# Kernel optimization log

Measured on AMD Instinct MI355X. Metric: run time of the kernel, lower is better.

The kernel has to match this reference:

```python
import jax, jax.numpy as jnp
import numpy as np

# Grid / solver constants (from init_kwargs)
N = 512        # grid is N x N
H = 1.0        # grid spacing h
IX, JX = 256, 256  # source cell indices
NITER = 1100   # Jacobi iterations; > 2*N so the wavefront fully converges
BIG = 1e10     # 'infinity' init for travel times


def setup_inputs() -> dict:
    key = jax.random.key(0)
    # positive slowness field in [0.5, 1.5)
    f = 0.5 + jax.random.uniform(key, (N, N), dtype=jnp.float32)
    return {"f": f}


def _solve(f):
    """Solve |grad u| = f with u(IX,JX)=0 via Godunov upwind Jacobi iteration.

    Each iteration applies the standard fast-sweeping local update in parallel
    to all cells and takes the pointwise min with the current u; this converges
    to the same viscosity-solution fixed point as sequential sweeping.
    """
    fh = f * H  # [N, N]
    u0 = jnp.full(f.shape, BIG, dtype=f.dtype).at[IX, JX].set(0.0)

    def step(u, _):
        up = jnp.pad(u, 1, constant_values=BIG)
        # one-sided upwind neighbor minima along each axis
        a = jnp.minimum(up[:-2, 1:-1], up[2:, 1:-1])   # i-direction
        b = jnp.minimum(up[1:-1, :-2], up[1:-1, 2:])   # j-direction
        d = jnp.abs(a - b)
        # Godunov update: 1D update if |a-b| >= f*h, else 2D quadratic root
        u_new = jnp.where(
            d >= fh,
            jnp.minimum(a, b) + fh,
            0.5 * (a + b + jnp.sqrt(jnp.maximum(2.0 * fh * fh - d * d, 0.0))),
        )
        u = jnp.minimum(u, u_new).at[IX, JX].set(0.0)
        return u, None

    u, _ = jax.lax.scan(jax.checkpoint(step), u0, None, length=NITER)
    return u


def reference(f):
    return _solve(f)
```

## Files before the change

### kernel.cpp

```cpp
#include <hip/hip_runtime.h>


#define NG     512
#define TS     16
#define BIGV   1e10f
#define SRC_I  256
#define SRC_J  256
#define KIN    16
#define ROUNDS 60
#define LSTR   24

#define GLB_LD(p)    __hip_atomic_load((p),      __ATOMIC_RELAXED, __HIP_MEMORY_SCOPE_AGENT)
#define GLB_ST(p, x) __hip_atomic_store((p), (x), __ATOMIC_RELAXED, __HIP_MEMORY_SCOPE_AGENT)

__device__ __forceinline__ float dpp_shr1(float x, float edge) {
    return __int_as_float(__builtin_amdgcn_update_dpp(
        __float_as_int(edge), __float_as_int(x), 0x111, 0xf, 0xf, false));
}
__device__ __forceinline__ float dpp_shl1(float x, float edge) {
    return __int_as_float(__builtin_amdgcn_update_dpp(
        __float_as_int(edge), __float_as_int(x), 0x101, 0xf, 0xf, false));
}

__global__ void eik_init(float* __restrict__ u) {
    int idx = blockIdx.x * blockDim.x + threadIdx.x;
    if (idx < NG * NG) u[idx] = (idx == SRC_I * NG + SRC_J) ? 0.0f : BIGV;
}

__global__ __launch_bounds__(128, 2) void eik_persist(const float* __restrict__ f,
                                                      float* __restrict__ u) {
    __shared__ float S[(TS + 2) * LSTR];

    const int tx = threadIdx.x;
    const int ty = threadIdx.y;
    const int r0 = 2 * ty;
    const int gi0  = blockIdx.y * TS + r0;
    const int gj   = blockIdx.x * TS + tx;
    const int base0 = gi0 * NG + gj;
    const int base1 = base0 + NG;

    const float fh0 = f[base0], fh1 = f[base1];
    const float fq0 = 2.0f * fh0 * fh0, fq1 = 2.0f * fh1 * fh1;

    float v0 = (gi0     == SRC_I && gj == SRC_J) ? 0.0f : BIGV;
    float v1 = (gi0 + 1 == SRC_I && gj == SRC_J) ? 0.0f : BIGV;

    const bool pn = (ty == 0), ps = (ty == TS / 2 - 1);
    const bool el = (tx == 0), er = (tx == TS - 1);
    const bool hast = (gi0 > 0), hasb = (gi0 + 2 < NG);
    const bool hasl = (gj > 0),  hasr = (gj + 1 < NG);

    const int aUP = (r0)     * LSTR + tx;
    const int aDN = (r0 + 3) * LSTR + tx;
    const int aW0 = (r0 + 1) * LSTR + tx;
    const int aW1 = (r0 + 2) * LSTR + tx;

    S[aW0] = v0;
    S[aW1] = v1;
    if (pn) S[0 * LSTR + tx] = BIGV;
    if (ps) S[(TS + 1) * LSTR + tx] = BIGV;
    __syncthreads();

#define UPD(vv, au, ad, lf, rt, fh_, fq_)                                   \
    do {                                                                    \
        float a  = fminf((au), (ad));                                       \
        float b  = fminf((lf), (rt));                                       \
        float s  = a - b;                                                   \
        float u1 = fminf(a, b) + (fh_);                                     \
        float t  = fmaf(-fabsf(s), fabsf(s), (fq_));         \
        float u2 = fmaf(0.5f, __builtin_amdgcn_sqrtf(t), 0.5f * (a + b));   \
        float un = (fabsf(s) >= (fh_)) ? u1 : u2;        \
        (vv) = fminf((vv), un);                                             \
    } while (0)

    for (int r = 0; r < ROUNDS; ++r) {
        float hW0 = BIGV, hW1 = BIGV, hE0 = BIGV, hE1 = BIGV;
        if (pn) S[0 * LSTR + tx] =
            hast ? GLB_LD(u + base0 - NG) : BIGV;
        if (ps) S[(TS + 1) * LSTR + tx] =
            hasb ? GLB_LD(u + base1 + NG) : BIGV;
        if (el && hasl) { hW0 = GLB_LD(u + base0 - 1);
                          hW1 = GLB_LD(u + base1 - 1); }
        if (er && hasr) { hE0 = GLB_LD(u + base0 + 1);
                          hE1 = GLB_LD(u + base1 + 1); }

        for (int it = 0; it < KIN; ++it) {
            const float up = S[aUP];
            const float dn = S[aDN];
            const float lf0 = dpp_shr1(v0, hW0), rt0 = dpp_shl1(v0, hE0);
            const float lf1 = dpp_shr1(v1, hW1), rt1 = dpp_shl1(v1, hE1);

            if ((it & 1) == 0) {
                UPD(v0, up, v1, lf0, rt0, fh0, fq0);
                UPD(v1, v0, dn, lf1, rt1, fh1, fq1);
            } else {
                UPD(v1, v0, dn, lf1, rt1, fh1, fq1);
                UPD(v0, up, v1, lf0, rt0, fh0, fq0);
            }

            S[aW0] = v0;
            S[aW1] = v1;
            __syncthreads();
        }

        if (pn) GLB_ST(u + base0, v0);
        if (ps) GLB_ST(u + base1, v1);
        if (el || er) { GLB_ST(u + base0, v0); GLB_ST(u + base1, v1); }
    }

    GLB_ST(u + base0, v0);
    GLB_ST(u + base1, v1);
#undef UPD
}

extern "C" void kernel_launch(void* const* d_in, const int* in_sizes, int n_in,
                              void* d_out, int out_size, void* d_ws, size_t ws_size,
                              hipStream_t stream) {
    const float* f = (const float*)d_in[0];
    float* u = (float*)d_out;

    eik_init<<<(NG * NG + 1023) / 1024, 1024, 0, stream>>>(u);

    dim3 grid(NG / TS, NG / TS);
    dim3 block(16, 8);
    eik_persist<<<grid, block, 0, stream>>>(f, u);
}
```

Baseline: 296.8 us.

## Halve workgroup barriers per round using atomic LDS accesses and lightweight sync

Replaces the per-iteration __syncthreads with one lightweight barrier per pair of inner iterations, and uses relaxed workgroup-scope atomic LDS loads and stores so rows read stale neighbour values in between. Each barrier is an explicit lgkmcnt wait plus s_barrier rather than a full fence. Rounds go from 60 to 62 to make up for the slower propagation across wave boundaries that the racy reads cause. The cost of barriers and fences is cut in exchange for non-deterministic intra-block data races that rely on the monotone min-update still converging.

```diff
diff --git a/kernel.cpp b/kernel.cpp
--- a/kernel.cpp
+++ b/kernel.cpp
@@ -7,11 +7,19 @@
 #define SRC_I  256
 #define SRC_J  256
 #define KIN    16
-#define ROUNDS 60
+#define ROUNDS 62
 #define LSTR   24
 
 #define GLB_LD(p)    __hip_atomic_load((p),      __ATOMIC_RELAXED, __HIP_MEMORY_SCOPE_AGENT)
 #define GLB_ST(p, x) __hip_atomic_store((p), (x), __ATOMIC_RELAXED, __HIP_MEMORY_SCOPE_AGENT)
+#define LDS_LD(p)    __hip_atomic_load((p),      __ATOMIC_RELAXED, __HIP_MEMORY_SCOPE_WORKGROUP)
+#define LDS_ST(p, x) __hip_atomic_store((p), (x), __ATOMIC_RELAXED, __HIP_MEMORY_SCOPE_WORKGROUP)
+
+#define SYNC()                                                  \
+    do {                                                        \
+        asm volatile("s_waitcnt lgkmcnt(0)" ::: "memory");      \
+        __builtin_amdgcn_s_barrier();                           \
+    } while (0)
 
 __device__ __forceinline__ float dpp_shr1(float x, float edge) {
     return __int_as_float(__builtin_amdgcn_update_dpp(
@@ -55,11 +63,13 @@
     const int aW0 = (r0 + 1) * LSTR + tx;
     const int aW1 = (r0 + 2) * LSTR + tx;
 
-    S[aW0] = v0;
-    S[aW1] = v1;
-    if (pn) S[0 * LSTR + tx] = BIGV;
-    if (ps) S[(TS + 1) * LSTR + tx] = BIGV;
+    LDS_ST(&S[aW0], v0);
+    LDS_ST(&S[aW1], v1);
+    if (pn) LDS_ST(&S[0 * LSTR + tx], BIGV);
+    if (ps) LDS_ST(&S[(TS + 1) * LSTR + tx], BIGV);
     __syncthreads();
+
+    float hW0 = BIGV, hW1 = BIGV, hE0 = BIGV, hE1 = BIGV;
 
 #define UPD(vv, au, ad, lf, rt, fh_, fq_)                                   \
     do {                                                                    \
@@ -73,35 +83,49 @@
         (vv) = fminf((vv), un);                                             \
     } while (0)
 
+#define ITER_PAIR()                                                         \
+    do {                                                                    \
+        {                           \
+            float up = LDS_LD(&S[aUP]);                                     \
+            float dn = LDS_LD(&S[aDN]);                                     \
+            float lf0 = dpp_shr1(v0, hW0), rt0 = dpp_shl1(v0, hE0);         \
+            float lf1 = dpp_shr1(v1, hW1), rt1 = dpp_shl1(v1, hE1);         \
+            UPD(v0, up, v1, lf0, rt0, fh0, fq0);                            \
+            UPD(v1, v0, dn, lf1, rt1, fh1, fq1);                            \
+            LDS_ST(&S[aW0], v0);                                            \
+            LDS_ST(&S[aW1], v1);                                            \
+        }                                                                   \
+        {                             \
+            float up = LDS_LD(&S[aUP]);                                     \
+            float dn = LDS_LD(&S[aDN]);                                     \
+            float lf0 = dpp_shr1(v0, hW0), rt0 = dpp_shl1(v0, hE0);         \
+            float lf1 = dpp_shr1(v1, hW1), rt1 = dpp_shl1(v1, hE1);         \
+            UPD(v1, v0, dn, lf1, rt1, fh1, fq1);                            \
+            UPD(v0, up, v1, lf0, rt0, fh0, fq0);                            \
+            LDS_ST(&S[aW0], v0);                                            \
+            LDS_ST(&S[aW1], v1);                                            \
+        }                                                                   \
+        SYNC();                                                             \
+    } while (0)
+
     for (int r = 0; r < ROUNDS; ++r) {
-        float hW0 = BIGV, hW1 = BIGV, hE0 = BIGV, hE1 = BIGV;
-        if (pn) S[0 * LSTR + tx] =
-            hast ? GLB_LD(u + base0 - NG) : BIGV;
-        if (ps) S[(TS + 1) * LSTR + tx] =
-            hasb ? GLB_LD(u + base1 + NG) : BIGV;
-        if (el && hasl) { hW0 = GLB_LD(u + base0 - 1);
-                          hW1 = GLB_LD(u + base1 - 1); }
-        if (er && hasr) { hE0 = GLB_LD(u + base0 + 1);
-                          hE1 = GLB_LD(u + base1 + 1); }
+        if (pn) LDS_ST(&S[0 * LSTR + tx],
+                       hast ? GLB_LD(u + base0 - NG) : BIGV);
+        if (ps) LDS_ST(&S[(TS + 1) * LSTR + tx],
+                       hasb ? GLB_LD(u + base1 + NG) : BIGV);
+        hW0 = (el && hasl) ? GLB_LD(u + base0 - 1) : BIGV;
+        hW1 = (el && hasl) ? GLB_LD(u + base1 - 1) : BIGV;
+        hE0 = (er && hasr) ? GLB_LD(u + base0 + 1) : BIGV;
+        hE1 = (er && hasr) ? GLB_LD(u + base1 + 1) : BIGV;
 
-        for (int it = 0; it < KIN; ++it) {
-            const float up = S[aUP];
-            const float dn = S[aDN];
-            const float lf0 = dpp_shr1(v0, hW0), rt0 = dpp_shl1(v0, hE0);
-            const float lf1 = dpp_shr1(v1, hW1), rt1 = dpp_shl1(v1, hE1);
-
-            if ((it & 1) == 0) {
-                UPD(v0, up, v1, lf0, rt0, fh0, fq0);
-                UPD(v1, v0, dn, lf1, rt1, fh1, fq1);
-            } else {
-                UPD(v1, v0, dn, lf1, rt1, fh1, fq1);
-                UPD(v0, up, v1, lf0, rt0, fh0, fq0);
-            }
-
-            S[aW0] = v0;
-            S[aW1] = v1;
-            __syncthreads();
-        }
+        ITER_PAIR();
+        ITER_PAIR();
+        ITER_PAIR();
+        ITER_PAIR();
+        ITER_PAIR();
+        ITER_PAIR();
+        ITER_PAIR();
+        ITER_PAIR();
 
         if (pn) GLB_ST(u + base0, v0);
         if (ps) GLB_ST(u + base1, v1);
@@ -110,6 +134,7 @@
 
     GLB_ST(u + base0, v0);
     GLB_ST(u + base1, v1);
+#undef ITER_PAIR
 #undef UPD
 }
 
```

After: 294.7 us. About the same (-0.7%).
